# Optimization experiments

Hardware: AMD Instinct MI355X
Metric: run time of the kernel (lower is better)

## Reference

```python
import jax, jax.numpy as jnp
import numpy as np
from jax import lax

D_TEMPORAL, D_INNER, D_STATE, D_CONV, DT_RANK = 2, 4, 16, 4, 1
EPS = 1e-5


def setup_inputs() -> dict:
    key = jax.random.key(0)
    ks = jax.random.split(key, 14)
    B, L = 16, 32768
    f = lambda k, s, scale=1.0: jax.random.normal(k, s, jnp.float32) * scale
    dt_b = float(np.log(np.expm1(0.01)))  # softplus^-1(0.01), typical dt init
    A_log = jnp.log(jnp.tile(jnp.arange(1, D_STATE + 1, dtype=jnp.float32), (D_INNER, 1)))
    return {
        "hidden_states": f(ks[0], (B, D_TEMPORAL, L)),
        "norm_w": jnp.ones((D_TEMPORAL,), jnp.float32),
        "in_proj_w": f(ks[1], (2 * D_INNER, D_TEMPORAL), 0.5),
        "conv_w": f(ks[2], (D_INNER, D_CONV), 0.3),
        "conv_b": f(ks[3], (D_INNER,), 0.1),
        "x_proj_w": f(ks[4], (DT_RANK + 2 * D_STATE, D_INNER), 0.3),
        "dt_proj_w": f(ks[5], (D_INNER, DT_RANK), 1.0),
        "dt_proj_b": jnp.full((D_INNER,), dt_b, jnp.float32),
        "A_log": A_log,
        "D": jnp.ones((D_INNER,), jnp.float32),
        "conv_w_b": f(ks[6], (D_INNER, D_CONV), 0.3),
        "conv_b_b": f(ks[7], (D_INNER,), 0.1),
        "x_proj_w_b": f(ks[8], (DT_RANK + 2 * D_STATE, D_INNER), 0.3),
        "dt_proj_w_b": f(ks[9], (D_INNER, DT_RANK), 1.0),
        "dt_proj_b_b": jnp.full((D_INNER,), dt_b, jnp.float32),
        "A_b_log": A_log,
        "D_b": jnp.ones((D_INNER,), jnp.float32),
        "out_proj_w": f(ks[10], (D_TEMPORAL, D_INNER), 0.3),
        "norm_f_w": jnp.ones((D_TEMPORAL,), jnp.float32),
    }


def _silu(x):
    return x * jax.nn.sigmoid(x)


def _rmsnorm(x, w):
    return x * lax.rsqrt(jnp.mean(x * x, axis=-1, keepdims=True) + EPS) * w


def _branch(x, z, conv_w, conv_b, x_proj_w, dt_proj_w, dt_proj_b, A_log, D):
    # x, z: (B, d_inner, L). Causal depthwise conv + silu.
    Bb, d, L = x.shape
    xc = lax.conv_general_dilated(
        x, conv_w[:, None, :], (1,), [(D_CONV - 1, 0)],
        feature_group_count=d, dimension_numbers=("NCH", "OIH", "NCH"))
    u = _silu(xc + conv_b[None, :, None]).transpose(0, 2, 1)      # (B, L, d)
    x_dbl = u @ x_proj_w.T                                        # (B, L, rank+2n)
    dt, Bm, Cm = jnp.split(x_dbl, [DT_RANK, DT_RANK + D_STATE], axis=-1)
    dt = jax.nn.softplus(dt @ dt_proj_w.T + dt_proj_b)            # (B, L, d)
    A = -jnp.exp(A_log)                                           # (d, n)
    dA = jnp.exp(dt[..., None] * A)                               # (B, L, d, n)
    dBu = (dt * u)[..., None] * Bm[:, :, None, :]                 # (B, L, d, n)

    def step(h, inp):
        dA_t, dBu_t, C_t = inp
        h = dA_t * h + dBu_t                                      # (B, d, n)
        return h, jnp.einsum("bdn,bn->bd", h, C_t)

    h0 = jnp.zeros((Bb, d, D_STATE), dtype=u.dtype)
    _, ys = lax.scan(step, h0, (jnp.swapaxes(dA, 0, 1), jnp.swapaxes(dBu, 0, 1), jnp.swapaxes(Cm, 0, 1)))
    y = jnp.swapaxes(ys, 0, 1) + u * D                            # (B, L, d)
    return y * _silu(z.transpose(0, 2, 1))


def _forward(hidden_states, norm_w, in_proj_w, conv_w, conv_b, x_proj_w, dt_proj_w,
             dt_proj_b, A_log, D, conv_w_b, conv_b_b, x_proj_w_b, dt_proj_w_b,
             dt_proj_b_b, A_b_log, D_b, out_proj_w, norm_f_w):
    # hidden_states: (B, T=d_temporal, L); scan runs over L.
    hs = jnp.swapaxes(hidden_states, 1, 2)                        # (B, L, T)
    residual = hs.astype(jnp.float32)
    hs = _rmsnorm(residual, norm_w)
    xz = jnp.swapaxes(hs @ in_proj_w.T, 1, 2)                     # (B, 2*d_inner, L)
    x, z = jnp.split(xz, 2, axis=1)
    y_f = _branch(x, z, conv_w, conv_b, x_proj_w, dt_proj_w, dt_proj_b, A_log, D)
    y_b = _branch(x[..., ::-1], z[..., ::-1], conv_w_b, conv_b_b, x_proj_w_b,
                  dt_proj_w_b, dt_proj_b_b, A_b_log, D_b)
    y = y_f + y_b[:, ::-1, :]                                     # (B, L, d_inner)
    out = y @ out_proj_w.T                                        # (B, L, T)
    out = _rmsnorm(out + residual, norm_f_w)
    return jnp.swapaxes(out, 1, 2)                                # (B, T, L)


def reference(hidden_states, norm_w, in_proj_w, conv_w, conv_b, x_proj_w, dt_proj_w,
              dt_proj_b, A_log, D, conv_w_b, conv_b_b, x_proj_w_b, dt_proj_w_b,
              dt_proj_b_b, A_b_log, D_b, out_proj_w, norm_f_w):
    return _forward(hidden_states, norm_w, in_proj_w, conv_w, conv_b, x_proj_w,
                    dt_proj_w, dt_proj_b, A_log, D, conv_w_b, conv_b_b, x_proj_w_b,
                    dt_proj_w_b, dt_proj_b_b, A_b_log, D_b, out_proj_w, norm_f_w)
```

## Files before the change

kernel.cpp:

```cpp
#include <hip/hip_runtime.h>
#include <cstdint>

#define BB 16
#define LL 32768
#define NC 512

#define WD_SZ 256
#define XPW 0
#define CVW 132
#define CVB 148
#define DTW 152
#define DTB 156
#define AW  160
#define DW  224
#define G_INPROJ 512
#define G_NORMW 528
#define G_OUTP 530
#define G_NORMF 538
#define FLG 1000

#define PQ_OFF 4096
#define PQ_BYTES ((size_t)BB*2*NC*64*8)
#define HIN_OFF (PQ_OFF + PQ_BYTES)

#define LOG2E 1.4426950408889634f

__device__ __forceinline__ float bf2f(unsigned short u){ return __uint_as_float(((unsigned int)u)<<16); }
__device__ __forceinline__ float blo(unsigned int u){ return __uint_as_float(u<<16); }
__device__ __forceinline__ float bhi(unsigned int u){ return __uint_as_float(u & 0xffff0000u); }

__device__ __forceinline__ unsigned int cvtpk(float lo, float hi){
  unsigned int r;
  asm("v_cvt_pk_bf16_f32 %0, %1, %2" : "=v"(r) : "v"(lo), "v"(hi));
  return r;
}
__device__ __forceinline__ unsigned short cvt1(float x){
  return (unsigned short)cvtpk(x, x);
}

__device__ __forceinline__ float siluf(float x){ return x / (1.f + __expf(-x)); }
__device__ __forceinline__ float softplusf_(float x){ return fmaxf(x,0.f) + log1pf(__expf(-fabsf(x))); }

__device__ __forceinline__ float exp2fast(float x){
#if __has_builtin(__builtin_amdgcn_exp2f)
  return __builtin_amdgcn_exp2f(x);
#else
  float r; asm("v_exp_f32 %0, %1\ns_nop 0" : "=v"(r) : "v"(x)); return r;
#endif
}

__device__ __forceinline__ float rowsum16(float x){
  asm("s_nop 1\n\t"
      "v_add_f32_dpp %0, %0, %0 row_ror:1 row_mask:0xf bank_mask:0xf\n\t"
      "s_nop 1\n\t"
      "v_add_f32_dpp %0, %0, %0 row_ror:2 row_mask:0xf bank_mask:0xf\n\t"
      "s_nop 1\n\t"
      "v_add_f32_dpp %0, %0, %0 row_ror:4 row_mask:0xf bank_mask:0xf\n\t"
      "s_nop 1\n\t"
      "v_add_f32_dpp %0, %0, %0 row_ror:8 row_mask:0xf bank_mask:0xf"
      : "+v"(x));
  return x;
}

__device__ __forceinline__ float ldw(const void* p, int i, int isf){
  return isf ? ((const float*)p)[i] : bf2f(((const unsigned short*)p)[i]);
}
__device__ __forceinline__ float2 hid2(const void* hid, int isf, int b, int t){
  if (isf){
    const float* p = (const float*)hid;
    return make_float2(p[(size_t)b*2*LL + t], p[(size_t)b*2*LL + LL + t]);
  }
  const unsigned short* p = (const unsigned short*)hid;
  return make_float2(bf2f(p[(size_t)b*2*LL + t]), bf2f(p[(size_t)b*2*LL + LL + t]));
}
__device__ __forceinline__ float4 xrow(const void* __restrict__ hid, int isf,
                                       const float* __restrict__ W, int b, int t){
  float2 h = hid2(hid, isf, b, t);
  float ms = rsqrtf(0.5f*(h.x*h.x + h.y*h.y) + 1e-5f);
  float v0 = h.x*ms*W[G_NORMW], v1 = h.y*ms*W[G_NORMW+1];
  float4 x;
  x.x = W[G_INPROJ+0]*v0 + W[G_INPROJ+1]*v1;
  x.y = W[G_INPROJ+2]*v0 + W[G_INPROJ+3]*v1;
  x.z = W[G_INPROJ+4]*v0 + W[G_INPROJ+5]*v1;
  x.w = W[G_INPROJ+6]*v0 + W[G_INPROJ+7]*v1;
  return x;
}

__global__ void k_prep(const void* __restrict__ normw, const void* __restrict__ inpj,
    const void* __restrict__ cwf, const void* __restrict__ cbf,
    const void* __restrict__ xpf, const void* __restrict__ dwf,
    const void* __restrict__ dbf, const void* __restrict__ alf,
    const void* __restrict__ ddf,
    const void* __restrict__ cwb, const void* __restrict__ cbb,
    const void* __restrict__ xpb, const void* __restrict__ dwb,
    const void* __restrict__ dbb, const void* __restrict__ alb,
    const void* __restrict__ ddb,
    const void* __restrict__ outp, const void* __restrict__ nfw,
    float* __restrict__ W)
{
  const int isf = (((const unsigned int*)ddf)[0] == 0x3F800000u) ? 1 : 0;
  int t = threadIdx.x;
  for (int i=t;i<132;i+=256){ W[XPW+i]=ldw(xpf,i,isf); W[WD_SZ+XPW+i]=ldw(xpb,i,isf); }
  for (int i=t;i<16;i+=256){ W[CVW+i]=ldw(cwf,i,isf); W[WD_SZ+CVW+i]=ldw(cwb,i,isf); W[G_INPROJ+i]=ldw(inpj,i,isf); }
  for (int i=t;i<4;i+=256){
    W[CVB+i]=ldw(cbf,i,isf); W[WD_SZ+CVB+i]=ldw(cbb,i,isf);
    W[DTW+i]=ldw(dwf,i,isf); W[WD_SZ+DTW+i]=ldw(dwb,i,isf);
    W[DTB+i]=ldw(dbf,i,isf); W[WD_SZ+DTB+i]=ldw(dbb,i,isf);
    W[DW+i] =ldw(ddf,i,isf); W[WD_SZ+DW+i] =ldw(ddb,i,isf);
  }
  for (int i=t;i<64;i+=256){
    W[AW+i]       = -__expf(ldw(alf,i,isf)) * LOG2E;
    W[WD_SZ+AW+i] = -__expf(ldw(alb,i,isf)) * LOG2E;
  }
  for (int i=t;i<8;i+=256) W[G_OUTP+i]=ldw(outp,i,isf);
  for (int i=t;i<2;i+=256){ W[G_NORMW+i]=ldw(normw,i,isf); W[G_NORMF+i]=ldw(nfw,i,isf); }
  if (t==0) W[FLG] = (float)isf;
}

template<int DR>
__device__ __forceinline__ float2 scan_chunk(const float (* __restrict__ dtPd)[68],
    const unsigned short (* __restrict__ dtud)[68],
    const unsigned short (* __restrict__ bpd)[68],
    float Ax, int d, int n)
{
  float P=1.f, Q=0.f;
  for (int j4=0; j4<16; j4++){
    const int t0 = DR ? 60-4*j4 : 4*j4;
    float4  d4 = *(const float4*)&dtPd[d][t0];
    ushort4 u4 = *(const ushort4*)&dtud[d][t0];
    ushort4 b4 = *(const ushort4*)&bpd[n][t0];
    float da[4]={d4.x,d4.y,d4.z,d4.w};
    unsigned short ua[4]={u4.x,u4.y,u4.z,u4.w};
    unsigned short ba[4]={b4.x,b4.y,b4.z,b4.w};
    #pragma unroll
    for (int jr=0; jr<4; jr++){
      const int k = DR ? 3-jr : jr;
      float e = exp2fast(Ax*da[k]);
      P *= e;
      Q = fmaf(Q, e, bf2f(ua[k])*bf2f(ba[k]));
    }
  }
  return make_float2(P,Q);
}

template<int DR>
__device__ __forceinline__ void scan_fused(const float (* __restrict__ dtPd)[68],
    const unsigned short (* __restrict__ dtud)[68],
    const unsigned int (* __restrict__ bcd)[68],
    float (* __restrict__ ySd)[68],
    float h, float Ax, int d, int n)
{
  for (int j4=0; j4<16; j4++){
    const int t0 = DR ? 60-4*j4 : 4*j4;
    float4  d4 = *(const float4*)&dtPd[d][t0];
    ushort4 u4 = *(const ushort4*)&dtud[d][t0];
    uint4   c4 = *(const uint4*)&bcd[n][t0];
    float da[4]={d4.x,d4.y,d4.z,d4.w};
    unsigned short ua[4]={u4.x,u4.y,u4.z,u4.w};
    unsigned int ca[4]={c4.x,c4.y,c4.z,c4.w};
    float s[4];
    #pragma unroll
    for (int jr=0; jr<4; jr++){
      const int k = DR ? 3-jr : jr;
      float e = exp2fast(Ax*da[k]);
      h = fmaf(e, h, bf2f(ua[k])*blo(ca[k]));
      s[k] = rowsum16(h*bhi(ca[k]));
    }
    if (n == 0) *(float4*)&ySd[d][t0] = make_float4(s[0],s[1],s[2],s[3]);
  }
}

__global__ __launch_bounds__(128, 4) void k_chunk(const void* __restrict__ hid,
    const float* __restrict__ W, float2* __restrict__ PQ)
{
  __shared__ __align__(16) float4 xb[70];
  __shared__ __align__(16) float dtP[2][4][68];
  __shared__ __align__(16) unsigned short dtuP[2][4][68];
  __shared__ __align__(16) unsigned short Bp[2][16][68];
  const int tid  = threadIdx.x;
  const int wid  = tid >> 6;
  const int lane = tid & 63;
  const int gid  = blockIdx.x;
  const int c    = gid & (NC-1);
  const int b    = gid >> 9;
  const int isf  = (int)W[FLG];

  if (wid == 0){
    int t = c*64 + lane;
    xb[lane+3] = xrow(hid, isf, W, b, t);
    if (lane < 3){
      int t2 = c*64 - 3 + lane;
      float4 v = make_float4(0.f,0.f,0.f,0.f);
      if (t2 >= 0) v = xrow(hid, isf, W, b, t2);
      xb[lane] = v;
    }
    if (lane >= 61){
      int t3 = c*64 + lane + 3;
      float4 v = make_float4(0.f,0.f,0.f,0.f);
      if (t3 < LL) v = xrow(hid, isf, W, b, t3);
      xb[lane+6] = v;
    }
  }
  __syncthreads();
  {
    const float* Wd = W + wid*WD_SZ;
    float4 a0,a1,a2,a3;
    if (wid == 0){ a0=xb[lane];   a1=xb[lane+1]; a2=xb[lane+2]; a3=xb[lane+3]; }
    else         { a0=xb[lane+6]; a1=xb[lane+5]; a2=xb[lane+4]; a3=xb[lane+3]; }
    float u[4];
    u[0] = siluf(Wd[CVB+0] + Wd[CVW+ 0]*a0.x + Wd[CVW+ 1]*a1.x + Wd[CVW+ 2]*a2.x + Wd[CVW+ 3]*a3.x);
    u[1] = siluf(Wd[CVB+1] + Wd[CVW+ 4]*a0.y + Wd[CVW+ 5]*a1.y + Wd[CVW+ 6]*a2.y + Wd[CVW+ 7]*a3.y);
    u[2] = siluf(Wd[CVB+2] + Wd[CVW+ 8]*a0.z + Wd[CVW+ 9]*a1.z + Wd[CVW+10]*a2.z + Wd[CVW+11]*a3.z);
    u[3] = siluf(Wd[CVB+3] + Wd[CVW+12]*a0.w + Wd[CVW+13]*a1.w + Wd[CVW+14]*a2.w + Wd[CVW+15]*a3.w);
    float dtr = Wd[XPW+0]*u[0] + Wd[XPW+1]*u[1] + Wd[XPW+2]*u[2] + Wd[XPW+3]*u[3];
    #pragma unroll
    for (int d2=0; d2<4; d2++){
      float dt = softplusf_(fmaf(Wd[DTW+d2], dtr, Wd[DTB+d2]));
      dtP[wid][d2][lane]  = dt;
      dtuP[wid][d2][lane] = cvt1(dt*u[d2]);
    }
    #pragma unroll
    for (int n=0; n<16; n++){
      float Bn = Wd[XPW+(1+n)*4+0]*u[0] + Wd[XPW+(1+n)*4+1]*u[1]
               + Wd[XPW+(1+n)*4+2]*u[2] + Wd[XPW+(1+n)*4+3]*u[3];
      Bp[wid][n][lane] = cvt1(Bn);
    }
  }
  __syncthreads();
  const int d = lane>>4, n = lane&15;
  const float Ax = W[wid*WD_SZ + AW + d*16 + n];
  float2 pq;
  size_t idx;
  if (wid == 0){
    pq  = scan_chunk<0>(dtP[0], dtuP[0], Bp[0], Ax, d, n);
    idx = ((size_t)(b*2+0)*NC + c);
  } else {
    pq  = scan_chunk<1>(dtP[1], dtuP[1], Bp[1], Ax, d, n);
    idx = ((size_t)(b*2+1)*NC + (NC-1-c));
  }
  PQ[idx*64 + lane] = pq;
}

#define SCAN_WAVES 8
#define SCAN_CPW (NC/SCAN_WAVES)
__global__ __launch_bounds__(512) void k_scan(const float2* __restrict__ PQ, float* __restrict__ hin)
{
  __shared__ float As[SCAN_WAVES][64];
  __shared__ float Bs[SCAN_WAVES][64];
  const int bd = blockIdx.x;
  const int lane = threadIdx.x & 63;
  const int w    = threadIdx.x >> 6;
  const size_t base = (size_t)bd*NC + (size_t)w*SCAN_CPW;
  float A = 1.f, Bc = 0.f;
  for (int c0=0; c0<SCAN_CPW; c0+=16){
    float2 v[16];
    #pragma unroll
    for (int k=0;k<16;k++) v[k] = PQ[(base+c0+k)*64 + lane];
    #pragma unroll
    for (int k=0;k<16;k++){ A *= v[k].x; Bc = fmaf(v[k].x, Bc, v[k].y); }
  }
  As[w][lane] = A; Bs[w][lane] = Bc;
  __syncthreads();
  float h = 0.f;
  for (int j=0;j<w;j++) h = fmaf(As[j][lane], h, Bs[j][lane]);
  for (int c0=0; c0<SCAN_CPW; c0+=16){
    float2 v[16];
    #pragma unroll
    for (int k=0;k<16;k++) v[k] = PQ[(base+c0+k)*64 + lane];
    #pragma unroll
    for (int k=0;k<16;k++){
      hin[(base+c0+k)*64 + lane] = h;
      h = fmaf(v[k].x, h, v[k].y);
    }
  }
}

__global__ __launch_bounds__(128, 4) void k_fused(const void* __restrict__ hid,
    const float* __restrict__ W, const float* __restrict__ hin,
    void* __restrict__ out)
{
  __shared__ __align__(16) char smx[2176];
  __shared__ __align__(16) float dtP[2][4][68];
  __shared__ __align__(16) unsigned short dtuP[2][4][68];
  __shared__ __align__(16) unsigned int BCp[2][16][68];
  __shared__ __align__(16) float zs[256];
  __shared__ __align__(16) float uD2[2][256];
  float4* xb = (float4*)smx;
  float (*yS)[4][68] = (float (*)[4][68])smx;

  const int tid  = threadIdx.x;
  const int wid  = tid >> 6;
  const int lane = tid & 63;
  const int gid  = blockIdx.x;
  const int c    = gid & (NC-1);
  const int b    = gid >> 9;
  const int isf  = (int)W[FLG];

  const int rc = wid ? (NC-1-c) : c;
  float h0 = hin[((size_t)(b*2+wid)*NC + rc)*64 + lane];

  if (wid == 0){
    int t = c*64 + lane;
    xb[lane+3] = xrow(hid, isf, W, b, t);
    if (lane < 3){
      int t2 = c*64 - 3 + lane;
      float4 v = make_float4(0.f,0.f,0.f,0.f);
      if (t2 >= 0) v = xrow(hid, isf, W, b, t2);
      xb[lane] = v;
    }
    if (lane >= 61){
      int t3 = c*64 + lane + 3;
      float4 v = make_float4(0.f,0.f,0.f,0.f);
      if (t3 < LL) v = xrow(hid, isf, W, b, t3);
      xb[lane+6] = v;
    }
  } else {
    int t = c*64 + lane;
    float2 hh = hid2(hid, isf, b, t);
    float ms = rsqrtf(0.5f*(hh.x*hh.x + hh.y*hh.y) + 1e-5f);
    float v0 = hh.x*ms*W[G_NORMW], v1 = hh.y*ms*W[G_NORMW+1];
    float4 z4;
    z4.x = siluf(W[G_INPROJ+ 8]*v0 + W[G_INPROJ+ 9]*v1);
    z4.y = siluf(W[G_INPROJ+10]*v0 + W[G_INPROJ+11]*v1);
    z4.z = siluf(W[G_INPROJ+12]*v0 + W[G_INPROJ+13]*v1);
    z4.w = siluf(W[G_INPROJ+14]*v0 + W[G_INPROJ+15]*v1);
    *(float4*)&zs[lane*4] = z4;
  }
  __syncthreads();
  {
    const float* Wd = W + wid*WD_SZ;
    float4 a0,a1,a2,a3;
    if (wid == 0){ a0=xb[lane];   a1=xb[lane+1]; a2=xb[lane+2]; a3=xb[lane+3]; }
    else         { a0=xb[lane+6]; a1=xb[lane+5]; a2=xb[lane+4]; a3=xb[lane+3]; }
    float u[4];
    u[0] = siluf(Wd[CVB+0] + Wd[CVW+ 0]*a0.x + Wd[CVW+ 1]*a1.x + Wd[CVW+ 2]*a2.x + Wd[CVW+ 3]*a3.x);
    u[1] = siluf(Wd[CVB+1] + Wd[CVW+ 4]*a0.y + Wd[CVW+ 5]*a1.y + Wd[CVW+ 6]*a2.y + Wd[CVW+ 7]*a3.y);
    u[2] = siluf(Wd[CVB+2] + Wd[CVW+ 8]*a0.z + Wd[CVW+ 9]*a1.z + Wd[CVW+10]*a2.z + Wd[CVW+11]*a3.z);
    u[3] = siluf(Wd[CVB+3] + Wd[CVW+12]*a0.w + Wd[CVW+13]*a1.w + Wd[CVW+14]*a2.w + Wd[CVW+15]*a3.w);
    float dtr = Wd[XPW+0]*u[0] + Wd[XPW+1]*u[1] + Wd[XPW+2]*u[2] + Wd[XPW+3]*u[3];
    float4 ud4;
    #pragma unroll
    for (int d2=0; d2<4; d2++){
      float dt = softplusf_(fmaf(Wd[DTW+d2], dtr, Wd[DTB+d2]));
      dtP[wid][d2][lane]  = dt;
      dtuP[wid][d2][lane] = cvt1(dt*u[d2]);
      ((float*)&ud4)[d2] = u[d2]*Wd[DW+d2];
    }
    *(float4*)&uD2[wid][lane*4] = ud4;
    #pragma unroll
    for (int n=0; n<16; n++){
      float Bn = Wd[XPW+(1+n)*4+0]*u[0] + Wd[XPW+(1+n)*4+1]*u[1]
               + Wd[XPW+(1+n)*4+2]*u[2] + Wd[XPW+(1+n)*4+3]*u[3];
      float Cn = Wd[XPW+(17+n)*4+0]*u[0] + Wd[XPW+(17+n)*4+1]*u[1]
               + Wd[XPW+(17+n)*4+2]*u[2] + Wd[XPW+(17+n)*4+3]*u[3];
      BCp[wid][n][lane] = cvtpk(Bn, Cn);
    }
  }
  __syncthreads();

  const int d = lane>>4, n = lane&15;
  const float Ax = W[wid*WD_SZ + AW + d*16 + n];
  if (wid == 0) scan_fused<0>(dtP[0], dtuP[0], BCp[0], yS[0], h0, Ax, d, n);
  else          scan_fused<1>(dtP[1], dtuP[1], BCp[1], yS[1], h0, Ax, d, n);
  __syncthreads();

  {
    int t = c*64 + lane;
    float4 zz = *(const float4*)&zs[lane*4];
    float4 u0 = *(const float4*)&uD2[0][lane*4];
    float4 u1 = *(const float4*)&uD2[1][lane*4];
    float y0 = (yS[0][0][lane] + yS[1][0][lane] + u0.x + u1.x) * zz.x;
    float y1 = (yS[0][1][lane] + yS[1][1][lane] + u0.y + u1.y) * zz.y;
    float y2 = (yS[0][2][lane] + yS[1][2][lane] + u0.z + u1.z) * zz.z;
    float y3 = (yS[0][3][lane] + yS[1][3][lane] + u0.w + u1.w) * zz.w;
    float o0 = W[G_OUTP+0]*y0 + W[G_OUTP+1]*y1 + W[G_OUTP+2]*y2 + W[G_OUTP+3]*y3;
    float o1 = W[G_OUTP+4]*y0 + W[G_OUTP+5]*y1 + W[G_OUTP+6]*y2 + W[G_OUTP+7]*y3;
    float2 r = hid2(hid, isf, b, t);
    o0 += r.x;
    o1 += r.y;
    float ms = rsqrtf(0.5f*(o0*o0 + o1*o1) + 1e-5f);
    float e0 = o0*ms*W[G_NORMF], e1 = o1*ms*W[G_NORMF+1];
    size_t i0 = (size_t)b*2*LL + t, i1 = i0 + LL;
    if (isf){
      if (wid == 0) ((float*)out)[i0] = e0;
      else          ((float*)out)[i1] = e1;
    } else {
      if (wid == 0) ((unsigned short*)out)[i0] = cvt1(e0);
      else          ((unsigned short*)out)[i1] = cvt1(e1);
    }
  }
}

extern "C" void kernel_launch(void* const* d_in, const int* in_sizes, int n_in,
                              void* d_out, int out_size, void* d_ws, size_t ws_size,
                              hipStream_t stream)
{
  (void)in_sizes; (void)n_in; (void)out_size; (void)ws_size;
  const void* hid   = d_in[0];
  const void* normw = d_in[1];
  const void* inpj  = d_in[2];
  const void* cwf   = d_in[3];
  const void* cbf   = d_in[4];
  const void* xpf   = d_in[5];
  const void* dwf   = d_in[6];
  const void* dbf   = d_in[7];
  const void* alf   = d_in[8];
  const void* ddf   = d_in[9];
  const void* cwb   = d_in[10];
  const void* cbb   = d_in[11];
  const void* xpb   = d_in[12];
  const void* dwb   = d_in[13];
  const void* dbb   = d_in[14];
  const void* alb   = d_in[15];
  const void* ddb   = d_in[16];
  const void* outp  = d_in[17];
  const void* nfw   = d_in[18];

  float* W   = (float*)d_ws;
  float2* PQ = (float2*)((char*)d_ws + PQ_OFF);
  float* hin = (float*)((char*)d_ws + HIN_OFF);

  k_prep<<<1,256,0,stream>>>(normw, inpj, cwf, cbf, xpf, dwf, dbf, alf, ddf,
                             cwb, cbb, xpb, dwb, dbb, alb, ddb, outp, nfw, W);
  k_chunk<<<BB*NC, 128, 0, stream>>>(hid, W, PQ);
  k_scan<<<BB*2, 512, 0, stream>>>(PQ, hin);
  k_fused<<<BB*NC, 128, 0, stream>>>(hid, W, hin, d_out);
}
```

Measured before the change: 194.0 us.

## Replace two-pass chunk scan with single pass plus stored state-correction weights

```diff
diff --git a/kernel.cpp b/kernel.cpp
--- a/kernel.cpp
+++ b/kernel.cpp
@@ -4,6 +4,8 @@
 #define BB 16
 #define LL 32768
 #define NC 512
+#define NSPAN 32
+#define SPLEN 16
 
 #define WD_SZ 256
 #define XPW 0
@@ -21,7 +23,12 @@
 
 #define PQ_OFF 4096
 #define PQ_BYTES ((size_t)BB*2*NC*64*8)
-#define HIN_OFF (PQ_OFF + PQ_BYTES)
+#define SP_OFF (PQ_OFF + PQ_BYTES)
+#define SP_BYTES ((size_t)BB*2*NSPAN*64*8)
+#define WG_OFF (SP_OFF + SP_BYTES)
+#define WG_BYTES ((size_t)BB*NC*2*64*64*2)
+#define YB_OFF (WG_OFF + WG_BYTES)
+#define YB_BYTES ((size_t)BB*NC*64*4*4)
 
 #define LOG2E 1.4426950408889634f
 
@@ -118,38 +125,16 @@
 }
 
 template<int DR>
-__device__ __forceinline__ float2 scan_chunk(const float (* __restrict__ dtPd)[68],
-    const unsigned short (* __restrict__ dtud)[68],
-    const unsigned short (* __restrict__ bpd)[68],
-    float Ax, int d, int n)
-{
-  float P=1.f, Q=0.f;
-  for (int j4=0; j4<16; j4++){
-    const int t0 = DR ? 60-4*j4 : 4*j4;
-    float4  d4 = *(const float4*)&dtPd[d][t0];
-    ushort4 u4 = *(const ushort4*)&dtud[d][t0];
-    ushort4 b4 = *(const ushort4*)&bpd[n][t0];
-    float da[4]={d4.x,d4.y,d4.z,d4.w};
-    unsigned short ua[4]={u4.x,u4.y,u4.z,u4.w};
-    unsigned short ba[4]={b4.x,b4.y,b4.z,b4.w};
-    #pragma unroll
-    for (int jr=0; jr<4; jr++){
-      const int k = DR ? 3-jr : jr;
-      float e = exp2fast(Ax*da[k]);
-      P *= e;
-      Q = fmaf(Q, e, bf2f(ua[k])*bf2f(ba[k]));
-    }
-  }
-  return make_float2(P,Q);
-}
-
-template<int DR>
-__device__ __forceinline__ void scan_fused(const float (* __restrict__ dtPd)[68],
+__device__ __forceinline__ float2 scan_store(const float (* __restrict__ dtPd)[68],
     const unsigned short (* __restrict__ dtud)[68],
     const unsigned int (* __restrict__ bcd)[68],
     float (* __restrict__ ySd)[68],
-    float h, float Ax, int d, int n)
-{
+    unsigned short* __restrict__ wrow,
+    float Ax, int d, int n, int dn)
+{
+  unsigned short* wr   = wrow + dn;
+  unsigned short* wrHi = wr + 32*64;
+  float P = 1.f, h = 0.f;
   for (int j4=0; j4<16; j4++){
     const int t0 = DR ? 60-4*j4 : 4*j4;
     float4  d4 = *(const float4*)&dtPd[d][t0];
@@ -161,22 +146,32 @@
     float s[4];
     #pragma unroll
     for (int jr=0; jr<4; jr++){
-      const int k = DR ? 3-jr : jr;
+      const int k  = DR ? 3-jr : jr;
+      const int tt = t0 + k;
       float e = exp2fast(Ax*da[k]);
+      P *= e;
+      float Cf = bhi(ca[k]);
       h = fmaf(e, h, bf2f(ua[k])*blo(ca[k]));
-      s[k] = rowsum16(h*bhi(ca[k]));
+      ((tt < 32) ? wr : wrHi)[(tt & 31)*64] = cvt1(P*Cf);
+      s[k] = rowsum16(h*Cf);
     }
     if (n == 0) *(float4*)&ySd[d][t0] = make_float4(s[0],s[1],s[2],s[3]);
   }
-}
-
-__global__ __launch_bounds__(128, 4) void k_chunk(const void* __restrict__ hid,
-    const float* __restrict__ W, float2* __restrict__ PQ)
-{
-  __shared__ __align__(16) float4 xb[70];
+  return make_float2(P, h);
+}
+
+__global__ __launch_bounds__(128, 4) void k_chunk2(const void* __restrict__ hid,
+    const float* __restrict__ W, float2* __restrict__ PQ,
+    unsigned short* __restrict__ Wg, float4* __restrict__ YB)
+{
+  __shared__ __align__(16) char smx[2176];
   __shared__ __align__(16) float dtP[2][4][68];
   __shared__ __align__(16) unsigned short dtuP[2][4][68];
-  __shared__ __align__(16) unsigned short Bp[2][16][68];
+  __shared__ __align__(16) unsigned int BCp[2][16][68];
+  __shared__ __align__(16) float uD[2][256];
+  float4* xb = (float4*)smx;
+  float (*yS)[4][68] = (float (*)[4][68])smx;
+
   const int tid  = threadIdx.x;
   const int wid  = tid >> 6;
   const int lane = tid & 63;
@@ -200,131 +195,6 @@
       if (t3 < LL) v = xrow(hid, isf, W, b, t3);
       xb[lane+6] = v;
     }
-  }
-  __syncthreads();
-  {
-    const float* Wd = W + wid*WD_SZ;
-    float4 a0,a1,a2,a3;
-    if (wid == 0){ a0=xb[lane];   a1=xb[lane+1]; a2=xb[lane+2]; a3=xb[lane+3]; }
-    else         { a0=xb[lane+6]; a1=xb[lane+5]; a2=xb[lane+4]; a3=xb[lane+3]; }
-    float u[4];
-    u[0] = siluf(Wd[CVB+0] + Wd[CVW+ 0]*a0.x + Wd[CVW+ 1]*a1.x + Wd[CVW+ 2]*a2.x + Wd[CVW+ 3]*a3.x);
-    u[1] = siluf(Wd[CVB+1] + Wd[CVW+ 4]*a0.y + Wd[CVW+ 5]*a1.y + Wd[CVW+ 6]*a2.y + Wd[CVW+ 7]*a3.y);
-    u[2] = siluf(Wd[CVB+2] + Wd[CVW+ 8]*a0.z + Wd[CVW+ 9]*a1.z + Wd[CVW+10]*a2.z + Wd[CVW+11]*a3.z);
-    u[3] = siluf(Wd[CVB+3] + Wd[CVW+12]*a0.w + Wd[CVW+13]*a1.w + Wd[CVW+14]*a2.w + Wd[CVW+15]*a3.w);
-    float dtr = Wd[XPW+0]*u[0] + Wd[XPW+1]*u[1] + Wd[XPW+2]*u[2] + Wd[XPW+3]*u[3];
-    #pragma unroll
-    for (int d2=0; d2<4; d2++){
-      float dt = softplusf_(fmaf(Wd[DTW+d2], dtr, Wd[DTB+d2]));
-      dtP[wid][d2][lane]  = dt;
-      dtuP[wid][d2][lane] = cvt1(dt*u[d2]);
-    }
-    #pragma unroll
-    for (int n=0; n<16; n++){
-      float Bn = Wd[XPW+(1+n)*4+0]*u[0] + Wd[XPW+(1+n)*4+1]*u[1]
-               + Wd[XPW+(1+n)*4+2]*u[2] + Wd[XPW+(1+n)*4+3]*u[3];
-      Bp[wid][n][lane] = cvt1(Bn);
-    }
-  }
-  __syncthreads();
-  const int d = lane>>4, n = lane&15;
-  const float Ax = W[wid*WD_SZ + AW + d*16 + n];
-  float2 pq;
-  size_t idx;
-  if (wid == 0){
-    pq  = scan_chunk<0>(dtP[0], dtuP[0], Bp[0], Ax, d, n);
-    idx = ((size_t)(b*2+0)*NC + c);
-  } else {
-    pq  = scan_chunk<1>(dtP[1], dtuP[1], Bp[1], Ax, d, n);
-    idx = ((size_t)(b*2+1)*NC + (NC-1-c));
-  }
-  PQ[idx*64 + lane] = pq;
-}
-
-#define SCAN_WAVES 8
-#define SCAN_CPW (NC/SCAN_WAVES)
-__global__ __launch_bounds__(512) void k_scan(const float2* __restrict__ PQ, float* __restrict__ hin)
-{
-  __shared__ float As[SCAN_WAVES][64];
-  __shared__ float Bs[SCAN_WAVES][64];
-  const int bd = blockIdx.x;
-  const int lane = threadIdx.x & 63;
-  const int w    = threadIdx.x >> 6;
-  const size_t base = (size_t)bd*NC + (size_t)w*SCAN_CPW;
-  float A = 1.f, Bc = 0.f;
-  for (int c0=0; c0<SCAN_CPW; c0+=16){
-    float2 v[16];
-    #pragma unroll
-    for (int k=0;k<16;k++) v[k] = PQ[(base+c0+k)*64 + lane];
-    #pragma unroll
-    for (int k=0;k<16;k++){ A *= v[k].x; Bc = fmaf(v[k].x, Bc, v[k].y); }
-  }
-  As[w][lane] = A; Bs[w][lane] = Bc;
-  __syncthreads();
-  float h = 0.f;
-  for (int j=0;j<w;j++) h = fmaf(As[j][lane], h, Bs[j][lane]);
-  for (int c0=0; c0<SCAN_CPW; c0+=16){
-    float2 v[16];
-    #pragma unroll
-    for (int k=0;k<16;k++) v[k] = PQ[(base+c0+k)*64 + lane];
-    #pragma unroll
-    for (int k=0;k<16;k++){
-      hin[(base+c0+k)*64 + lane] = h;
-      h = fmaf(v[k].x, h, v[k].y);
-    }
-  }
-}
-
-__global__ __launch_bounds__(128, 4) void k_fused(const void* __restrict__ hid,
-    const float* __restrict__ W, const float* __restrict__ hin,
-    void* __restrict__ out)
-{
-  __shared__ __align__(16) char smx[2176];
-  __shared__ __align__(16) float dtP[2][4][68];
-  __shared__ __align__(16) unsigned short dtuP[2][4][68];
-  __shared__ __align__(16) unsigned int BCp[2][16][68];
-  __shared__ __align__(16) float zs[256];
-  __shared__ __align__(16) float uD2[2][256];
-  float4* xb = (float4*)smx;
-  float (*yS)[4][68] = (float (*)[4][68])smx;
-
-  const int tid  = threadIdx.x;
-  const int wid  = tid >> 6;
-  const int lane = tid & 63;
-  const int gid  = blockIdx.x;
-  const int c    = gid & (NC-1);
-  const int b    = gid >> 9;
-  const int isf  = (int)W[FLG];
-
-  const int rc = wid ? (NC-1-c) : c;
-  float h0 = hin[((size_t)(b*2+wid)*NC + rc)*64 + lane];
-
-  if (wid == 0){
-    int t = c*64 + lane;
-    xb[lane+3] = xrow(hid, isf, W, b, t);
-    if (lane < 3){
-      int t2 = c*64 - 3 + lane;
-      float4 v = make_float4(0.f,0.f,0.f,0.f);
-      if (t2 >= 0) v = xrow(hid, isf, W, b, t2);
-      xb[lane] = v;
-    }
-    if (lane >= 61){
-      int t3 = c*64 + lane + 3;
-      float4 v = make_float4(0.f,0.f,0.f,0.f);
-      if (t3 < LL) v = xrow(hid, isf, W, b, t3);
-      xb[lane+6] = v;
-    }
-  } else {
-    int t = c*64 + lane;
-    float2 hh = hid2(hid, isf, b, t);
-    float ms = rsqrtf(0.5f*(hh.x*hh.x + hh.y*hh.y) + 1e-5f);
-    float v0 = hh.x*ms*W[G_NORMW], v1 = hh.y*ms*W[G_NORMW+1];
-    float4 z4;
-    z4.x = siluf(W[G_INPROJ+ 8]*v0 + W[G_INPROJ+ 9]*v1);
-    z4.y = siluf(W[G_INPROJ+10]*v0 + W[G_INPROJ+11]*v1);
-    z4.z = siluf(W[G_INPROJ+12]*v0 + W[G_INPROJ+13]*v1);
-    z4.w = siluf(W[G_INPROJ+14]*v0 + W[G_INPROJ+15]*v1);
-    *(float4*)&zs[lane*4] = z4;
   }
   __syncthreads();
   {
@@ -346,7 +216,7 @@
       dtuP[wid][d2][lane] = cvt1(dt*u[d2]);
       ((float*)&ud4)[d2] = u[d2]*Wd[DW+d2];
     }
-    *(float4*)&uD2[wid][lane*4] = ud4;
+    *(float4*)&uD[wid][lane*4] = ud4;
     #pragma unroll
     for (int n=0; n<16; n++){
       float Bn = Wd[XPW+(1+n)*4+0]*u[0] + Wd[XPW+(1+n)*4+1]*u[1]
@@ -360,33 +230,149 @@
 
   const int d = lane>>4, n = lane&15;
   const float Ax = W[wid*WD_SZ + AW + d*16 + n];
-  if (wid == 0) scan_fused<0>(dtP[0], dtuP[0], BCp[0], yS[0], h0, Ax, d, n);
-  else          scan_fused<1>(dtP[1], dtuP[1], BCp[1], yS[1], h0, Ax, d, n);
+  unsigned short* wrow = Wg + ((size_t)gid*2 + wid)*64*64;
+  float2 pq;
+  size_t idx;
+  if (wid == 0){
+    pq  = scan_store<0>(dtP[0], dtuP[0], BCp[0], yS[0], wrow, Ax, d, n, lane);
+    idx = ((size_t)(b*2+0)*NC + c);
+  } else {
+    pq  = scan_store<1>(dtP[1], dtuP[1], BCp[1], yS[1], wrow, Ax, d, n, lane);
+    idx = ((size_t)(b*2+1)*NC + (NC-1-c));
+  }
+  PQ[idx*64 + lane] = pq;
   __syncthreads();
 
+  if (wid == 0){
+    float4 v;
+    v.x = yS[0][0][lane] + yS[1][0][lane] + uD[0][lane*4+0] + uD[1][lane*4+0];
+    v.y = yS[0][1][lane] + yS[1][1][lane] + uD[0][lane*4+1] + uD[1][lane*4+1];
+    v.z = yS[0][2][lane] + yS[1][2][lane] + uD[0][lane*4+2] + uD[1][lane*4+2];
+    v.w = yS[0][3][lane] + yS[1][3][lane] + uD[0][lane*4+3] + uD[1][lane*4+3];
+    YB[(size_t)gid*64 + lane] = v;
+  }
+}
+
+__global__ __launch_bounds__(64) void k_spans(const float2* __restrict__ PQ,
+                                              float2* __restrict__ SP)
+{
+  const int blk  = blockIdx.x;
+  const int lane = threadIdx.x;
+  const int bd   = blk >> 5, span = blk & (NSPAN-1);
+  const float2* p = PQ + ((size_t)bd*NC + span*SPLEN)*64 + lane;
+  float2 v[SPLEN];
+  #pragma unroll
+  for (int k=0;k<SPLEN;k++) v[k] = p[k*64];
+  float A = 1.f, Bc = 0.f;
+  #pragma unroll
+  for (int k=0;k<SPLEN;k++){ A *= v[k].x; Bc = fmaf(v[k].x, Bc, v[k].y); }
+  SP[((size_t)bd*NSPAN + span)*64 + lane] = make_float2(A,Bc);
+}
+
+__device__ __forceinline__ float dot16(uint4 q0, uint4 q1, const float* h){
+  float4 h0 = *(const float4*)(h+0),  h1 = *(const float4*)(h+4);
+  float4 h2 = *(const float4*)(h+8),  h3 = *(const float4*)(h+12);
+  float cacc = 0.f;
+  cacc = fmaf(blo(q0.x), h0.x, cacc); cacc = fmaf(bhi(q0.x), h0.y, cacc);
+  cacc = fmaf(blo(q0.y), h0.z, cacc); cacc = fmaf(bhi(q0.y), h0.w, cacc);
+  cacc = fmaf(blo(q0.z), h1.x, cacc); cacc = fmaf(bhi(q0.z), h1.y, cacc);
+  cacc = fmaf(blo(q0.w), h1.z, cacc); cacc = fmaf(bhi(q0.w), h1.w, cacc);
+  cacc = fmaf(blo(q1.x), h2.x, cacc); cacc = fmaf(bhi(q1.x), h2.y, cacc);
+  cacc = fmaf(blo(q1.y), h2.z, cacc); cacc = fmaf(bhi(q1.y), h2.w, cacc);
+  cacc = fmaf(blo(q1.z), h3.x, cacc); cacc = fmaf(bhi(q1.z), h3.y, cacc);
+  cacc = fmaf(blo(q1.w), h3.z, cacc); cacc = fmaf(bhi(q1.w), h3.w, cacc);
+  return cacc;
+}
+
+__global__ __launch_bounds__(64) void k_final(const void* __restrict__ hid,
+    const float* __restrict__ W, const float2* __restrict__ PQ,
+    const float2* __restrict__ SP, const unsigned short* __restrict__ Wg,
+    const float4* __restrict__ YB, void* __restrict__ out)
+{
+  __shared__ float h0s[2][64];
+  const int lane = threadIdx.x;
+  const int gid  = blockIdx.x;
+  const int c    = gid & (NC-1);
+  const int b    = gid >> 9;
+  const int isf  = (int)W[FLG];
+
+  #pragma unroll
+  for (int dir=0; dir<2; dir++){
+    const int p  = dir ? (NC-1-c) : c;
+    const int bd = b*2 + dir;
+    const int s  = p >> 4, wn = p & 15;
+    const float2* SPb = SP + (size_t)bd*NSPAN*64 + lane;
+    const float2* PQb = PQ + ((size_t)bd*NC + (p & ~15))*64 + lane;
+    float h = 0.f;
+    #pragma unroll
+    for (int jg=0; jg<4; jg++){
+      if (jg*8 < s){
+        float2 v[8];
+        #pragma unroll
+        for (int j=0;j<8;j++){ int jj = jg*8+j; v[j] = SPb[(size_t)(jj<s?jj:0)*64]; }
+        #pragma unroll
+        for (int j=0;j<8;j++){ int jj = jg*8+j; if (jj<s) h = fmaf(v[j].x, h, v[j].y); }
+      }
+    }
+    #pragma unroll
+    for (int jg=0; jg<2; jg++){
+      if (jg*8 < wn){
+        float2 v[8];
+        #pragma unroll
+        for (int j=0;j<8;j++){ int jj = jg*8+j; v[j] = PQb[(size_t)(jj<wn?jj:0)*64]; }
+        #pragma unroll
+        for (int j=0;j<8;j++){ int jj = jg*8+j; if (jj<wn) h = fmaf(v[j].x, h, v[j].y); }
+      }
+    }
+    h0s[dir][lane] = h;
+  }
+  __syncthreads();
+
   {
-    int t = c*64 + lane;
-    float4 zz = *(const float4*)&zs[lane*4];
-    float4 u0 = *(const float4*)&uD2[0][lane*4];
-    float4 u1 = *(const float4*)&uD2[1][lane*4];
-    float y0 = (yS[0][0][lane] + yS[1][0][lane] + u0.x + u1.x) * zz.x;
-    float y1 = (yS[0][1][lane] + yS[1][1][lane] + u0.y + u1.y) * zz.y;
-    float y2 = (yS[0][2][lane] + yS[1][2][lane] + u0.z + u1.z) * zz.z;
-    float y3 = (yS[0][3][lane] + yS[1][3][lane] + u0.w + u1.w) * zz.w;
+    const int t = lane;
+    const uint4* wrF = (const uint4*)(Wg + (((size_t)gid*2 + 0)*64 + t)*64);
+    const uint4* wrB = (const uint4*)(Wg + (((size_t)gid*2 + 1)*64 + t)*64);
+    uint4 wf[8], wb[8];
+    #pragma unroll
+    for (int q=0;q<8;q++) wf[q] = wrF[q];
+    #pragma unroll
+    for (int q=0;q<8;q++) wb[q] = wrB[q];
+    float4 yb = YB[(size_t)gid*64 + t];
+
+    float corr[4];
+    #pragma unroll
+    for (int d2=0; d2<4; d2++){
+      float cf = dot16(wf[d2*2], wf[d2*2+1], &h0s[0][d2*16]);
+      float cb = dot16(wb[d2*2], wb[d2*2+1], &h0s[1][d2*16]);
+      corr[d2] = cf + cb;
+    }
+
+    const int tg = c*64 + t;
+    float2 r = hid2(hid, isf, b, tg);
+    float ms0 = rsqrtf(0.5f*(r.x*r.x + r.y*r.y) + 1e-5f);
+    float v0 = r.x*ms0*W[G_NORMW], v1 = r.y*ms0*W[G_NORMW+1];
+    float z0 = siluf(W[G_INPROJ+ 8]*v0 + W[G_INPROJ+ 9]*v1);
+    float z1 = siluf(W[G_INPROJ+10]*v0 + W[G_INPROJ+11]*v1);
+    float z2 = siluf(W[G_INPROJ+12]*v0 + W[G_INPROJ+13]*v1);
+    float z3 = siluf(W[G_INPROJ+14]*v0 + W[G_INPROJ+15]*v1);
+
+    float y0 = (yb.x + corr[0]) * z0;
+    float y1 = (yb.y + corr[1]) * z1;
+    float y2 = (yb.z + corr[2]) * z2;
+    float y3 = (yb.w + corr[3]) * z3;
     float o0 = W[G_OUTP+0]*y0 + W[G_OUTP+1]*y1 + W[G_OUTP+2]*y2 + W[G_OUTP+3]*y3;
     float o1 = W[G_OUTP+4]*y0 + W[G_OUTP+5]*y1 + W[G_OUTP+6]*y2 + W[G_OUTP+7]*y3;
-    float2 r = hid2(hid, isf, b, t);
     o0 += r.x;
     o1 += r.y;
     float ms = rsqrtf(0.5f*(o0*o0 + o1*o1) + 1e-5f);
     float e0 = o0*ms*W[G_NORMF], e1 = o1*ms*W[G_NORMF+1];
-    size_t i0 = (size_t)b*2*LL + t, i1 = i0 + LL;
+    size_t i0 = (size_t)b*2*LL + tg, i1 = i0 + LL;
     if (isf){
-      if (wid == 0) ((float*)out)[i0] = e0;
-      else          ((float*)out)[i1] = e1;
+      ((float*)out)[i0] = e0;
+      ((float*)out)[i1] = e1;
     } else {
-      if (wid == 0) ((unsigned short*)out)[i0] = cvt1(e0);
-      else          ((unsigned short*)out)[i1] = cvt1(e1);
+      ((unsigned short*)out)[i0] = cvt1(e0);
+      ((unsigned short*)out)[i1] = cvt1(e1);
     }
   }
 }
@@ -416,13 +402,15 @@
   const void* outp  = d_in[17];
   const void* nfw   = d_in[18];
 
-  float* W   = (float*)d_ws;
-  float2* PQ = (float2*)((char*)d_ws + PQ_OFF);
-  float* hin = (float*)((char*)d_ws + HIN_OFF);
+  float* W            = (float*)d_ws;
+  float2* PQ          = (float2*)((char*)d_ws + PQ_OFF);
+  float2* SPt         = (float2*)((char*)d_ws + SP_OFF);
+  unsigned short* Wg  = (unsigned short*)((char*)d_ws + WG_OFF);
+  float4* YB          = (float4*)((char*)d_ws + YB_OFF);
 
   k_prep<<<1,256,0,stream>>>(normw, inpj, cwf, cbf, xpf, dwf, dbf, alf, ddf,
                              cwb, cbb, xpb, dwb, dbb, alb, ddb, outp, nfw, W);
-  k_chunk<<<BB*NC, 128, 0, stream>>>(hid, W, PQ);
-  k_scan<<<BB*2, 512, 0, stream>>>(PQ, hin);
-  k_fused<<<BB*NC, 128, 0, stream>>>(hid, W, hin, d_out);
-}
+  k_chunk2<<<BB*NC, 128, 0, stream>>>(hid, W, PQ, Wg, YB);
+  k_spans<<<BB*2*NSPAN, 64, 0, stream>>>(PQ, SPt);
+  k_final<<<BB*NC, 64, 0, stream>>>(hid, W, PQ, SPt, Wg, YB, d_out);
+}
```

Result: no change. 196.6 us (+1.3%).
